# Kernel tuning notes

Measured on AMD Instinct MI355X. Metric: run time of the kernel, lower is better.

The kernel has to match this reference:

```python
import jax, jax.numpy as jnp
import numpy as np

N_CAPS, R, CIN, COUT = 10, 1152, 8, 16  # digit caps, primary caps (32*6*6), caps dims
B = 256


def setup_inputs() -> dict:
    key = jax.random.key(0)
    k1, k2 = jax.random.split(key)
    x = jax.random.normal(k1, (B, R, CIN), dtype=jnp.float32)
    # learned transform W: [num_capsules, num_route_nodes, in_channels, out_channels]
    W = jax.random.normal(k2, (N_CAPS, R, CIN, COUT), dtype=jnp.float32)
    return {"x": x, "W": W}


def squash(t, axis=-1):
    sq = jnp.sum(t * t, axis=axis, keepdims=True)
    return sq / (1.0 + sq) * t / jnp.sqrt(sq)


def reference(x, W):
    # u_hat = (x[None,:,:,None,:] @ W[:,None]) -> [N_CAPS, B, R, 1, COUT]; squeeze the 1.
    u_hat = jnp.einsum('bri,nrio->nbro', x, W)  # [N, B, R, O]
    # NOTE: the original forward returns v_j INSIDE the routing loop, so exactly one
    # iteration executes: b_ij = 0 => c_ij = softmax(zeros, dim=route) = 1/R (uniform).
    c = 1.0 / u_hat.shape[2]
    s = jnp.sum(c * u_hat, axis=2, keepdims=True)  # [N, B, 1, O]
    v = squash(s, axis=-1)
    return v[:, :, :, None, :]  # [N, B, 1, 1, O] to match torch v_j shape
```

## Files before the change

### kernel.cpp

```cpp
#include <hip/hip_runtime.h>

#define B_SZ 256
#define RNODES 1152
#define CIN 8
#define COUT 16
#define NCAPS 10
#define KDIM (RNODES*CIN)
#define NCOL (NCAPS*COUT)
#define WSTRIDE (KDIM*COUT)

#define LROW 40
#define XROWS 64
#define WOFF (XROWS*LROW)
#define BUFSZ (WOFF + NCOL*LROW)

using bf16x8 = __attribute__((ext_vector_type(8))) short;
using f32x4  = __attribute__((ext_vector_type(4))) float;

__device__ __forceinline__ unsigned short f2bf(float f) {
  unsigned int u = __builtin_bit_cast(unsigned int, f);
  u += 0x7FFFu + ((u >> 16) & 1u);
  return (unsigned short)(u >> 16);
}

__global__ __launch_bounds__(256) void caps_gemm(const float* __restrict__ x,
                                                 const float* __restrict__ W,
                                                 float* __restrict__ ws) {
  __shared__ unsigned short lds[2][BUFSZ];
  const int tid = threadIdx.x;
  const int bid = blockIdx.x;
  const int mt  = bid & 3;
  const int ks  = bid >> 2;
  const int b0  = mt * 64;

  int step0, nsteps;
  if (ks < 32) { step0 = ks * 5;              nsteps = 5; }
  else         { step0 = 160 + (ks - 32) * 4; nsteps = 4; }
  const int k0 = step0 * 32;

  const int xrow0 = tid >> 3;
  const int xf4   = (tid & 7) * 4;

  f32x4 acc[NCAPS];
#pragma unroll
  for (int i = 0; i < NCAPS; ++i) acc[i] = (f32x4){0.f, 0.f, 0.f, 0.f};

  float4 px[2];
  float4 pw[5];

  {
    const int kg = k0;
#pragma unroll
    for (int j = 0; j < 2; ++j) {
      const int row = xrow0 + j * 32;
      px[j] = *(const float4*)(x + (size_t)(b0 + row) * KDIM + kg + xf4);
    }
#pragma unroll
    for (int j = 0; j < 5; ++j) {
      const int idx = tid + 256 * j;
      const int c4 = idx >> 5, kl = idx & 31;
      const int n = c4 >> 2, o4 = (c4 & 3) << 2;
      pw[j] = *(const float4*)(W + (size_t)n * WSTRIDE + (size_t)(kg + kl) * COUT + o4);
    }
  }

  const int lane = tid & 63;
  const int wv   = tid >> 6;
  const int q    = lane >> 4;
  const int m16  = lane & 15;
  const int a_off = (wv * 16 + m16) * LROW + q * 8;

  for (int s = 0; s < nsteps; ++s) {
    unsigned short* buf = lds[s & 1];

#pragma unroll
    for (int j = 0; j < 2; ++j) {
      const int row = xrow0 + j * 32;
      ushort4 v;
      v.x = f2bf(px[j].x); v.y = f2bf(px[j].y);
      v.z = f2bf(px[j].z); v.w = f2bf(px[j].w);
      *(ushort4*)&buf[row * LROW + xf4] = v;
    }
#pragma unroll
    for (int j = 0; j < 5; ++j) {
      const int idx = tid + 256 * j;
      const int c4 = idx >> 5, kl = idx & 31;
      const int n = c4 >> 2, o4 = (c4 & 3) << 2;
      const int cbase = WOFF + (n * COUT + o4) * LROW + kl;
      buf[cbase + 0 * LROW] = f2bf(pw[j].x);
      buf[cbase + 1 * LROW] = f2bf(pw[j].y);
      buf[cbase + 2 * LROW] = f2bf(pw[j].z);
      buf[cbase + 3 * LROW] = f2bf(pw[j].w);
    }
    __syncthreads();

    if (s + 1 < nsteps) {
      const int kg = k0 + (s + 1) * 32;
#pragma unroll
      for (int j = 0; j < 2; ++j) {
        const int row = xrow0 + j * 32;
        px[j] = *(const float4*)(x + (size_t)(b0 + row) * KDIM + kg + xf4);
      }
#pragma unroll
      for (int j = 0; j < 5; ++j) {
        const int idx = tid + 256 * j;
        const int c4 = idx >> 5, kl = idx & 31;
        const int n = c4 >> 2, o4 = (c4 & 3) << 2;
        pw[j] = *(const float4*)(W + (size_t)n * WSTRIDE + (size_t)(kg + kl) * COUT + o4);
      }
    }

    bf16x8 a = *(const bf16x8*)&buf[a_off];
#pragma unroll
    for (int nt = 0; nt < NCAPS; ++nt) {
      bf16x8 bfrag = *(const bf16x8*)&buf[WOFF + (nt * COUT + m16) * LROW + q * 8];
      acc[nt] = __builtin_amdgcn_mfma_f32_16x16x32_bf16(a, bfrag, acc[nt], 0, 0, 0);
    }
  }

  const int brow = b0 + wv * 16 + q * 4;
#pragma unroll
  for (int nt = 0; nt < NCAPS; ++nt) {
#pragma unroll
    for (int r = 0; r < 4; ++r) {
      atomicAdd(&ws[((nt << 8) + (brow + r)) * COUT + m16], acc[nt][r]);
    }
  }
}

__global__ __launch_bounds__(256) void caps_squash(const float* __restrict__ ws,
                                                   float* __restrict__ out) {
  const int idx = blockIdx.x * 256 + threadIdx.x;
  float s = ws[idx] * (1.0f / (float)RNODES);
  float sq = s * s;
  sq += __shfl_xor(sq, 1);
  sq += __shfl_xor(sq, 2);
  sq += __shfl_xor(sq, 4);
  sq += __shfl_xor(sq, 8);
  out[idx] = s * sqrtf(sq) / (1.0f + sq);
}

extern "C" void kernel_launch(void* const* d_in, const int* in_sizes, int n_in,
                              void* d_out, int out_size, void* d_ws, size_t ws_size,
                              hipStream_t stream) {
  const float* x = (const float*)d_in[0];
  const float* W = (const float*)d_in[1];
  float* ws  = (float*)d_ws;
  float* out = (float*)d_out;

  hipMemsetAsync(ws, 0, NCAPS * B_SZ * COUT * sizeof(float), stream);
  caps_gemm<<<dim3(256), dim3(256), 0, stream>>>(x, W, ws);
  caps_squash<<<dim3(NCAPS * B_SZ * COUT / 256), dim3(256), 0, stream>>>(ws, out);
}
```

Baseline: 76.76 us.

## Replace atomic split-K with partial buffers, more splits, and direct A-fragment loads

Raises the split-K factor to 96 slices across 384 blocks, each issuing all of its W and x global loads up front for three K steps. The A fragments are now converted straight from registers instead of being staged through LDS. Per-block partial sums are written to a workspace and summed by a separate reduce-plus-squash kernel, which removes the memset and the float atomics. The cost is about 15 MB of partial-sum traffic through the workspace and higher register pressure from holding all prefetched loads at once.

```diff
diff --git a/kernel.cpp b/kernel.cpp
--- a/kernel.cpp
+++ b/kernel.cpp
@@ -2,17 +2,16 @@
 
 #define B_SZ 256
 #define RNODES 1152
-#define CIN 8
+#define KDIM 9216
 #define COUT 16
 #define NCAPS 10
-#define KDIM (RNODES*CIN)
-#define NCOL (NCAPS*COUT)
 #define WSTRIDE (KDIM*COUT)
 
 #define LROW 40
-#define XROWS 64
-#define WOFF (XROWS*LROW)
-#define BUFSZ (WOFF + NCOL*LROW)
+#define WBUF (NCAPS*COUT*LROW)
+#define STEPS 3
+#define SPLITS 96
+#define PARTL 10240
 
 using bf16x8 = __attribute__((ext_vector_type(8))) short;
 using f32x4  = __attribute__((ext_vector_type(4))) float;
@@ -26,118 +25,105 @@
 __global__ __launch_bounds__(256) void caps_gemm(const float* __restrict__ x,
                                                  const float* __restrict__ W,
                                                  float* __restrict__ ws) {
-  __shared__ unsigned short lds[2][BUFSZ];
+  __shared__ unsigned short wbuf[STEPS][WBUF];
   const int tid = threadIdx.x;
   const int bid = blockIdx.x;
+  const int ks  = bid >> 2;
   const int mt  = bid & 3;
-  const int ks  = bid >> 2;
   const int b0  = mt * 64;
+  const int k0  = ks * (STEPS * 32);
 
-  int step0, nsteps;
-  if (ks < 32) { step0 = ks * 5;              nsteps = 5; }
-  else         { step0 = 160 + (ks - 32) * 4; nsteps = 4; }
-  const int k0 = step0 * 32;
+  const int lane = tid & 63;
+  const int wv   = tid >> 6;
+  const int q    = lane >> 4;
+  const int m16  = lane & 15;
 
-  const int xrow0 = tid >> 3;
-  const int xf4   = (tid & 7) * 4;
+  const int c4 = tid >> 5;
+  const int kl = tid & 31;
+  float4 pw[STEPS][5];
+#pragma unroll
+  for (int s = 0; s < STEPS; ++s)
+#pragma unroll
+    for (int j = 0; j < 5; ++j) {
+      const int cc = c4 + 8 * j;
+      const int n  = cc >> 2, o4 = (cc & 3) << 2;
+      pw[s][j] = *(const float4*)(W + (size_t)n * WSTRIDE +
+                                  (size_t)(k0 + s * 32 + kl) * COUT + o4);
+    }
+
+  const float* xrow = x + (size_t)(b0 + wv * 16 + m16) * KDIM + k0 + q * 8;
+  float4 pa[STEPS][2];
+#pragma unroll
+  for (int s = 0; s < STEPS; ++s) {
+    pa[s][0] = *(const float4*)(xrow + s * 32);
+    pa[s][1] = *(const float4*)(xrow + s * 32 + 4);
+  }
 
   f32x4 acc[NCAPS];
 #pragma unroll
   for (int i = 0; i < NCAPS; ++i) acc[i] = (f32x4){0.f, 0.f, 0.f, 0.f};
 
-  float4 px[2];
-  float4 pw[5];
-
-  {
-    const int kg = k0;
 #pragma unroll
-    for (int j = 0; j < 2; ++j) {
-      const int row = xrow0 + j * 32;
-      px[j] = *(const float4*)(x + (size_t)(b0 + row) * KDIM + kg + xf4);
-    }
+  for (int s = 0; s < STEPS; ++s) {
 #pragma unroll
     for (int j = 0; j < 5; ++j) {
-      const int idx = tid + 256 * j;
-      const int c4 = idx >> 5, kl = idx & 31;
-      const int n = c4 >> 2, o4 = (c4 & 3) << 2;
-      pw[j] = *(const float4*)(W + (size_t)n * WSTRIDE + (size_t)(kg + kl) * COUT + o4);
+      const int cc = c4 + 8 * j;
+      const int n  = cc >> 2, o4 = (cc & 3) << 2;
+      const int cb = (n * COUT + o4) * LROW + kl;
+      unsigned short* b = &wbuf[s][0];
+      b[cb + 0 * LROW] = f2bf(pw[s][j].x);
+      b[cb + 1 * LROW] = f2bf(pw[s][j].y);
+      b[cb + 2 * LROW] = f2bf(pw[s][j].z);
+      b[cb + 3 * LROW] = f2bf(pw[s][j].w);
+    }
+    __syncthreads();
+
+    bf16x8 a;
+    a[0] = (short)f2bf(pa[s][0].x); a[1] = (short)f2bf(pa[s][0].y);
+    a[2] = (short)f2bf(pa[s][0].z); a[3] = (short)f2bf(pa[s][0].w);
+    a[4] = (short)f2bf(pa[s][1].x); a[5] = (short)f2bf(pa[s][1].y);
+    a[6] = (short)f2bf(pa[s][1].z); a[7] = (short)f2bf(pa[s][1].w);
+#pragma unroll
+    for (int nt = 0; nt < NCAPS; ++nt) {
+      bf16x8 bf = *(const bf16x8*)&wbuf[s][(nt * COUT + m16) * LROW + q * 8];
+      acc[nt] = __builtin_amdgcn_mfma_f32_16x16x32_bf16(a, bf, acc[nt], 0, 0, 0);
     }
   }
 
-  const int lane = tid & 63;
-  const int wv   = tid >> 6;
-  const int q    = lane >> 4;
-  const int m16  = lane & 15;
-  const int a_off = (wv * 16 + m16) * LROW + q * 8;
-
-  for (int s = 0; s < nsteps; ++s) {
-    unsigned short* buf = lds[s & 1];
-
+  float* P = ws + (size_t)bid * PARTL;
+  const int br = wv * 16 + q * 4;
 #pragma unroll
-    for (int j = 0; j < 2; ++j) {
-      const int row = xrow0 + j * 32;
-      ushort4 v;
-      v.x = f2bf(px[j].x); v.y = f2bf(px[j].y);
-      v.z = f2bf(px[j].z); v.w = f2bf(px[j].w);
-      *(ushort4*)&buf[row * LROW + xf4] = v;
-    }
+  for (int nt = 0; nt < NCAPS; ++nt)
 #pragma unroll
-    for (int j = 0; j < 5; ++j) {
-      const int idx = tid + 256 * j;
-      const int c4 = idx >> 5, kl = idx & 31;
-      const int n = c4 >> 2, o4 = (c4 & 3) << 2;
-      const int cbase = WOFF + (n * COUT + o4) * LROW + kl;
-      buf[cbase + 0 * LROW] = f2bf(pw[j].x);
-      buf[cbase + 1 * LROW] = f2bf(pw[j].y);
-      buf[cbase + 2 * LROW] = f2bf(pw[j].z);
-      buf[cbase + 3 * LROW] = f2bf(pw[j].w);
-    }
-    __syncthreads();
-
-    if (s + 1 < nsteps) {
-      const int kg = k0 + (s + 1) * 32;
-#pragma unroll
-      for (int j = 0; j < 2; ++j) {
-        const int row = xrow0 + j * 32;
-        px[j] = *(const float4*)(x + (size_t)(b0 + row) * KDIM + kg + xf4);
-      }
-#pragma unroll
-      for (int j = 0; j < 5; ++j) {
-        const int idx = tid + 256 * j;
-        const int c4 = idx >> 5, kl = idx & 31;
-        const int n = c4 >> 2, o4 = (c4 & 3) << 2;
-        pw[j] = *(const float4*)(W + (size_t)n * WSTRIDE + (size_t)(kg + kl) * COUT + o4);
-      }
-    }
-
-    bf16x8 a = *(const bf16x8*)&buf[a_off];
-#pragma unroll
-    for (int nt = 0; nt < NCAPS; ++nt) {
-      bf16x8 bfrag = *(const bf16x8*)&buf[WOFF + (nt * COUT + m16) * LROW + q * 8];
-      acc[nt] = __builtin_amdgcn_mfma_f32_16x16x32_bf16(a, bfrag, acc[nt], 0, 0, 0);
-    }
-  }
-
-  const int brow = b0 + wv * 16 + q * 4;
-#pragma unroll
-  for (int nt = 0; nt < NCAPS; ++nt) {
-#pragma unroll
-    for (int r = 0; r < 4; ++r) {
-      atomicAdd(&ws[((nt << 8) + (brow + r)) * COUT + m16], acc[nt][r]);
-    }
-  }
+    for (int r = 0; r < 4; ++r)
+      P[nt * 1024 + (br + r) * COUT + m16] = acc[nt][r];
 }
 
-__global__ __launch_bounds__(256) void caps_squash(const float* __restrict__ ws,
+__global__ __launch_bounds__(256) void caps_reduce(const float* __restrict__ ws,
                                                    float* __restrict__ out) {
-  const int idx = blockIdx.x * 256 + threadIdx.x;
-  float s = ws[idx] * (1.0f / (float)RNODES);
+  const int tid = threadIdx.x;
+  const int mt  = blockIdx.x & 3;
+  const int seg = blockIdx.x >> 2;
+  const int L   = seg * 256 + tid;
+
+  const float* p = ws + (size_t)mt * PARTL + L;
+  float s0 = 0.f, s1 = 0.f, s2 = 0.f, s3 = 0.f;
+#pragma unroll 4
+  for (int ks = 0; ks < SPLITS; ks += 4) {
+    s0 += p[(size_t)(ks + 0) * (4 * PARTL)];
+    s1 += p[(size_t)(ks + 1) * (4 * PARTL)];
+    s2 += p[(size_t)(ks + 2) * (4 * PARTL)];
+    s3 += p[(size_t)(ks + 3) * (4 * PARTL)];
+  }
+  float s = ((s0 + s1) + (s2 + s3)) * (1.0f / (float)RNODES);
+
   float sq = s * s;
   sq += __shfl_xor(sq, 1);
   sq += __shfl_xor(sq, 2);
   sq += __shfl_xor(sq, 4);
   sq += __shfl_xor(sq, 8);
-  out[idx] = s * sqrtf(sq) / (1.0f + sq);
+  const int n = L >> 10, rem = L & 1023;
+  out[n * 4096 + mt * 1024 + rem] = s * sqrtf(sq) / (1.0f + sq);
 }
 
 extern "C" void kernel_launch(void* const* d_in, const int* in_sizes, int n_in,
@@ -148,7 +134,6 @@
   float* ws  = (float*)d_ws;
   float* out = (float*)d_out;
 
-  hipMemsetAsync(ws, 0, NCAPS * B_SZ * COUT * sizeof(float), stream);
-  caps_gemm<<<dim3(256), dim3(256), 0, stream>>>(x, W, ws);
-  caps_squash<<<dim3(NCAPS * B_SZ * COUT / 256), dim3(256), 0, stream>>>(ws, out);
+  caps_gemm<<<dim3(SPLITS * 4), dim3(256), 0, stream>>>(x, W, ws);
+  caps_reduce<<<dim3(160), dim3(256), 0, stream>>>(ws, out);
 }
```

Result: no change. 77.48 us (+0.9%).
